# Optimization experiments

Measured on AMD Instinct MI355X. Metric: run time of the kernel, lower is better.

## Reference

```python
import jax, jax.numpy as jnp
import numpy as np

B, C, H, W = 4, 256, 64, 64
OUT_C = 256
K = 3          # kernel_size
P = K // 2     # zero padding
EPS = 1e-5     # F.layer_norm default eps


def setup_inputs() -> dict:
    key = jax.random.key(0)
    ks = jax.random.split(key, 9)
    s = 0.02
    return {
        "x":  jax.random.normal(ks[0], (B, C, H, W), dtype=jnp.float32),
        "Wq": jax.random.normal(ks[1], (C, C), dtype=jnp.float32) * s,
        "bq": jax.random.normal(ks[2], (C,), dtype=jnp.float32) * s,
        "Wk": jax.random.normal(ks[3], (C, C), dtype=jnp.float32) * s,
        "bk": jax.random.normal(ks[4], (C,), dtype=jnp.float32) * s,
        "Wv": jax.random.normal(ks[5], (C, C), dtype=jnp.float32) * s,
        "bv": jax.random.normal(ks[6], (C,), dtype=jnp.float32) * s,
        "Wo": jax.random.normal(ks[7], (OUT_C, C), dtype=jnp.float32) * s,
        "bo": jax.random.normal(ks[8], (OUT_C,), dtype=jnp.float32) * s,
    }


def _forward(x, Wq, bq, Wk, bk, Wv, bv, Wo, bo):
    # LayerNorm over the last two dims [H, W], no affine (per (b, c) plane).
    mu = jnp.mean(x, axis=(2, 3), keepdims=True)
    var = jnp.var(x, axis=(2, 3), keepdims=True)
    xn = (x - mu) * jax.lax.rsqrt(var + EPS)

    xh = jnp.transpose(xn, (0, 2, 3, 1))            # [B, H, W, C]
    scale = jnp.asarray(C, xh.dtype) ** -0.5        # depth_scale = C**-0.5

    # Query only at each center pixel (only the center output is kept).
    q = (xh @ Wq.T + bq) * scale                    # [B, H, W, C]

    # Zero-pad the normalized input, then project: padded positions get K=bk, V=bv
    # exactly as torch's Linear applied to zero-padded windows.
    xp = jnp.pad(xh, ((0, 0), (P, P), (P, P), (0, 0)))  # [B, H+2P, W+2P, C]
    Kp = xp @ Wk.T + bk
    Vp = xp @ Wv.T + bv

    # Gather the K*K neighborhood for every pixel (small fixed loop over 9 shifts).
    Kw = jnp.stack([Kp[:, i:i + H, j:j + W, :] for i in range(K) for j in range(K)], axis=3)  # [B,H,W,9,C]
    Vw = jnp.stack([Vp[:, i:i + H, j:j + W, :] for i in range(K) for j in range(K)], axis=3)  # [B,H,W,9,C]

    logits = jnp.einsum('bhwc,bhwnc->bhwn', q, Kw)  # [B, H, W, 9]
    attn = jax.nn.softmax(logits, axis=-1)
    ctx = jnp.einsum('bhwn,bhwnc->bhwc', attn, Vw)  # [B, H, W, C]

    out = ctx @ Wo.T + bo                           # [B, H, W, OUT_C]
    return jnp.transpose(out, (0, 3, 1, 2))         # [B, OUT_C, H, W]


def reference(x, Wq, bq, Wk, bk, Wv, bv, Wo, bo):
    return _forward(x, Wq, bq, Wk, bk, Wv, bv, Wo, bo)
```

## Files before the change

kernel.cpp:

```cpp
#include <hip/hip_runtime.h>

typedef unsigned short u16;
typedef unsigned int   u32;

typedef __attribute__((ext_vector_type(4))) float f32x4;
typedef __attribute__((ext_vector_type(8))) short bf16x8;

#define HWDIM 4096
#define CDIM  256

__device__ __forceinline__ float bf2f(u16 u) { return __uint_as_float(((u32)u) << 16); }
__device__ __forceinline__ u16 f2bf(float f) {
    u32 u = __float_as_uint(f);
    u32 r = (u + 0x7fffu + ((u >> 16) & 1u)) >> 16;
    return (u16)r;
}

__global__ __launch_bounds__(256) void fill_kernel(float* __restrict__ out, int n) {
    int i = blockIdx.x * 256 + threadIdx.x;
    if (i < n) out[i] = 1.0f;
}

__global__ __launch_bounds__(256) void wconv_kernel(const float* __restrict__ s0,
                                                    const float* __restrict__ s1,
                                                    const float* __restrict__ s2,
                                                    const float* __restrict__ s3,
                                                    u16* __restrict__ d0, u16* __restrict__ d1,
                                                    u16* __restrict__ d2, u16* __restrict__ d3) {
    const float* s; u16* d;
    switch (blockIdx.y) {
        case 0: s = s0; d = d0; break;
        case 1: s = s1; d = d1; break;
        case 2: s = s2; d = d2; break;
        default: s = s3; d = d3; break;
    }
    int i = (blockIdx.x * 256 + threadIdx.x) * 4;
    float4 f = *(const float4*)(s + i);
    u16 tmp[4] = {f2bf(f.x), f2bf(f.y), f2bf(f.z), f2bf(f.w)};
    *(uint2*)(d + i) = *(uint2*)tmp;
}

__global__ __launch_bounds__(256) void ln_stats_kernel(const float* __restrict__ x,
                                                       float2* __restrict__ stats) {
    int plane = blockIdx.x;
    int t = threadIdx.x;
    const float* px = x + (size_t)plane * HWDIM;
    float sum = 0.f, ss = 0.f;
#pragma unroll
    for (int it = 0; it < 4; ++it) {
        float4 v = *(const float4*)(px + (t + it * 256) * 4);
        sum += v.x + v.y + v.z + v.w;
        ss  += v.x * v.x + v.y * v.y + v.z * v.z + v.w * v.w;
    }
#pragma unroll
    for (int o = 32; o; o >>= 1) { sum += __shfl_xor(sum, o); ss += __shfl_xor(ss, o); }
    __shared__ float s1[4], s2[4];
    int wid = t >> 6, lane = t & 63;
    if (lane == 0) { s1[wid] = sum; s2[wid] = ss; }
    __syncthreads();
    if (t == 0) {
        float S = s1[0] + s1[1] + s1[2] + s1[3];
        float Q = s2[0] + s2[1] + s2[2] + s2[3];
        float mu  = S * (1.f / HWDIM);
        float var = Q * (1.f / HWDIM) - mu * mu;
        stats[plane] = make_float2(mu, rsqrtf(var + 1e-5f));
    }
}

__global__ __launch_bounds__(256) void ln_transpose_kernel(const float* __restrict__ x,
                                                           const float2* __restrict__ stats,
                                                           u16* __restrict__ xh) {
    __shared__ __align__(16) u16 tile[64 * 72];
    int b  = blockIdx.z;
    int c0 = blockIdx.y * 64;
    int p0 = blockIdx.x * 64;
    int t  = threadIdx.x;
    int c_loc = t >> 2;
    int pc    = (t & 3) * 16;
    int plane = b * CDIM + c0 + c_loc;
    float2 st = stats[plane];
    const float* px = x + (size_t)plane * HWDIM + p0 + pc;
#pragma unroll
    for (int j2 = 0; j2 < 4; j2++) {
        float4 v = *(const float4*)(px + j2 * 4);
        int p = pc + j2 * 4;
        tile[(p + 0) * 72 + c_loc] = f2bf((v.x - st.x) * st.y);
        tile[(p + 1) * 72 + c_loc] = f2bf((v.y - st.x) * st.y);
        tile[(p + 2) * 72 + c_loc] = f2bf((v.z - st.x) * st.y);
        tile[(p + 3) * 72 + c_loc] = f2bf((v.w - st.x) * st.y);
    }
    __syncthreads();
    int cc = (t & 7) * 8;
#pragma unroll
    for (int it = 0; it < 2; ++it) {
        int p_loc = (t >> 3) + it * 32;
        uint4 val = *(uint4*)&tile[p_loc * 72 + cc];
        *(uint4*)(xh + ((size_t)(b * HWDIM + p0 + p_loc)) * CDIM + c0 + cc) = val;
    }
}

__device__ __forceinline__ void gemm_mainloop(const u16* __restrict__ A,
                                              const u16* __restrict__ Bm,
                                              u16* lA, u16* lB,
                                              f32x4 acc[4][4],
                                              int m0, int n0,
                                              int waveM, int waveN, int lane, int t) {
    int fr = lane & 15, kq = (lane >> 4) * 8;
    for (int k0 = 0; k0 < 256; k0 += 32) {
        int m1 = t >> 2, kc = (t & 3) * 8;
        int m2 = m1 + 64;
        *(uint4*)&lA[m1 * 32 + kc] = *(const uint4*)&A[(size_t)(m0 + m1) * 256 + k0 + kc];
        *(uint4*)&lA[m2 * 32 + kc] = *(const uint4*)&A[(size_t)(m0 + m2) * 256 + k0 + kc];
        *(uint4*)&lB[m1 * 32 + kc] = *(const uint4*)&Bm[(size_t)(n0 + m1) * 256 + k0 + kc];
        *(uint4*)&lB[m2 * 32 + kc] = *(const uint4*)&Bm[(size_t)(n0 + m2) * 256 + k0 + kc];
        __syncthreads();
        bf16x8 af[4], bfr[4];
#pragma unroll
        for (int i = 0; i < 4; i++) af[i]  = *(const bf16x8*)&lA[(waveM * 64 + i * 16 + fr) * 32 + kq];
#pragma unroll
        for (int j = 0; j < 4; j++) bfr[j] = *(const bf16x8*)&lB[(waveN * 64 + j * 16 + fr) * 32 + kq];
#pragma unroll
        for (int i = 0; i < 4; i++)
#pragma unroll
            for (int j = 0; j < 4; j++)
                acc[i][j] = __builtin_amdgcn_mfma_f32_16x16x32_bf16(af[i], bfr[j], acc[i][j], 0, 0, 0);
        __syncthreads();
    }
}

__global__ __launch_bounds__(256) void gemm_qkv_kernel(const u16* __restrict__ xh,
    const u16* __restrict__ Wq, const float* __restrict__ bq,
    const u16* __restrict__ Wk, const float* __restrict__ bk,
    const u16* __restrict__ Wv, const float* __restrict__ bv,
    u16* __restrict__ qo, u16* __restrict__ ko, u16* __restrict__ vo) {
    __shared__ __align__(16) u16 lA[128 * 32];
    __shared__ __align__(16) u16 lB[128 * 32];
    int t = threadIdx.x, lane = t & 63, wid = t >> 6;
    int waveM = wid >> 1, waveN = wid & 1;
    int mb = blockIdx.x, nb = blockIdx.y;
    const u16* W; const float* bias; u16* out; float scale = 1.f;
    int wsel = nb >> 1;
    if (wsel == 0)      { W = Wq; bias = bq; out = qo; scale = 0.0625f; }
    else if (wsel == 1) { W = Wk; bias = bk; out = ko; }
    else                { W = Wv; bias = bv; out = vo; }
    int n0 = (nb & 1) * 128;
    int m0 = mb * 128;
    f32x4 acc[4][4];
#pragma unroll
    for (int i = 0; i < 4; i++)
#pragma unroll
        for (int j = 0; j < 4; j++) acc[i][j] = (f32x4){0.f, 0.f, 0.f, 0.f};
    gemm_mainloop(xh, W, lA, lB, acc, m0, n0, waveM, waveN, lane, t);
    int fr = lane & 15, r0 = (lane >> 4) * 4;
#pragma unroll
    for (int j = 0; j < 4; j++) {
        int ng = n0 + waveN * 64 + j * 16 + fr;
        float bval = bias[ng];
#pragma unroll
        for (int i = 0; i < 4; i++) {
            int mrow = m0 + waveM * 64 + i * 16 + r0;
#pragma unroll
            for (int r = 0; r < 4; r++) {
                float vv = (acc[i][j][r] + bval) * scale;
                out[(size_t)(mrow + r) * 256 + ng] = f2bf(vv);
            }
        }
    }
}

__global__ __launch_bounds__(256) void attn_kernel(const u16* __restrict__ q,
                                                   const u16* __restrict__ kb,
                                                   const u16* __restrict__ vb,
                                                   const float* __restrict__ bkf,
                                                   const float* __restrict__ bvf,
                                                   u16* __restrict__ ctx) {
    int t = threadIdx.x, wid = t >> 6, lane = t & 63;
    int pix = blockIdx.x * 4 + wid;
    int h = (pix >> 6) & 63, w = pix & 63;
    int c4 = lane << 2;
    uint2 qr = *(const uint2*)(q + (size_t)pix * 256 + c4);
    float q0 = __uint_as_float(qr.x << 16), q1 = __uint_as_float(qr.x & 0xffff0000u);
    float q2 = __uint_as_float(qr.y << 16), q3 = __uint_as_float(qr.y & 0xffff0000u);
    float4 kbias = *(const float4*)(bkf + c4);
    float4 vbias = *(const float4*)(bvf + c4);
    float part[9];
    int off[9];
#pragma unroll
    for (int n = 0; n < 9; n++) {
        int dy = n / 3 - 1, dx = n % 3 - 1;
        int hh = h + dy, ww = w + dx;
        bool inb = ((unsigned)hh < 64u) && ((unsigned)ww < 64u);
        off[n] = inb ? ((pix + dy * 64 + dx) << 8) : -1;
        float k0, k1, k2, k3;
        if (off[n] >= 0) {
            uint2 kr = *(const uint2*)(kb + off[n] + c4);
            k0 = __uint_as_float(kr.x << 16); k1 = __uint_as_float(kr.x & 0xffff0000u);
            k2 = __uint_as_float(kr.y << 16); k3 = __uint_as_float(kr.y & 0xffff0000u);
        } else {
            k0 = kbias.x; k1 = kbias.y; k2 = kbias.z; k3 = kbias.w;
        }
        part[n] = q0 * k0 + q1 * k1 + q2 * k2 + q3 * k3;
    }
#pragma unroll
    for (int o = 32; o; o >>= 1) {
#pragma unroll
        for (int n = 0; n < 9; n++) part[n] += __shfl_xor(part[n], o);
    }
    float m = part[0];
#pragma unroll
    for (int n = 1; n < 9; n++) m = fmaxf(m, part[n]);
    float e[9], s = 0.f;
#pragma unroll
    for (int n = 0; n < 9; n++) { e[n] = __expf(part[n] - m); s += e[n]; }
    float inv = 1.f / s;
    float a0 = 0.f, a1 = 0.f, a2 = 0.f, a3 = 0.f;
#pragma unroll
    for (int n = 0; n < 9; n++) {
        float v0, v1, v2, v3;
        if (off[n] >= 0) {
            uint2 vr = *(const uint2*)(vb + off[n] + c4);
            v0 = __uint_as_float(vr.x << 16); v1 = __uint_as_float(vr.x & 0xffff0000u);
            v2 = __uint_as_float(vr.y << 16); v3 = __uint_as_float(vr.y & 0xffff0000u);
        } else {
            v0 = vbias.x; v1 = vbias.y; v2 = vbias.z; v3 = vbias.w;
        }
        float wn = e[n] * inv;
        a0 += wn * v0; a1 += wn * v1; a2 += wn * v2; a3 += wn * v3;
    }
    u32 lo = (u32)f2bf(a0) | ((u32)f2bf(a1) << 16);
    u32 hi = (u32)f2bf(a2) | ((u32)f2bf(a3) << 16);
    *(uint2*)(ctx + (size_t)pix * 256 + c4) = make_uint2(lo, hi);
}

__global__ __launch_bounds__(256) void gemm_out_kernel(const u16* __restrict__ ctx,
                                                       const u16* __restrict__ Wo,
                                                       const float* __restrict__ bo,
                                                       float* __restrict__ out) {
    __shared__ __align__(16) u16 lA[128 * 32];
    __shared__ __align__(16) u16 lB[128 * 32];
    int t = threadIdx.x, lane = t & 63, wid = t >> 6;
    int waveM = wid >> 1, waveN = wid & 1;
    int m0 = blockIdx.x * 128;
    int n0 = blockIdx.y * 128;
    f32x4 acc[4][4];
#pragma unroll
    for (int i = 0; i < 4; i++)
#pragma unroll
        for (int j = 0; j < 4; j++) acc[i][j] = (f32x4){0.f, 0.f, 0.f, 0.f};
    gemm_mainloop(ctx, Wo, lA, lB, acc, m0, n0, waveM, waveN, lane, t);
    int fr = lane & 15, r0 = (lane >> 4) * 4;
#pragma unroll
    for (int j = 0; j < 4; j++) {
        int ng = n0 + waveN * 64 + j * 16 + fr;
        float bval = bo[ng];
#pragma unroll
        for (int i = 0; i < 4; i++) {
            int m = m0 + waveM * 64 + i * 16 + r0;
            int bidx = m >> 12;
            int p = m & 4095;
            float4 vv = make_float4(acc[i][j][0] + bval, acc[i][j][1] + bval,
                                    acc[i][j][2] + bval, acc[i][j][3] + bval);
            *(float4*)(out + ((size_t)(bidx * 256 + ng)) * HWDIM + p) = vv;
        }
    }
}

extern "C" void kernel_launch(void* const* d_in, const int* in_sizes, int n_in,
                              void* d_out, int out_size, void* d_ws, size_t ws_size,
                              hipStream_t stream) {
    const float* x  = (const float*)d_in[0];
    const float* Wq = (const float*)d_in[1];
    const float* bq = (const float*)d_in[2];
    const float* Wk = (const float*)d_in[3];
    const float* bk = (const float*)d_in[4];
    const float* Wv = (const float*)d_in[5];
    const float* bv = (const float*)d_in[6];
    const float* Wo = (const float*)d_in[7];
    const float* bo = (const float*)d_in[8];
    float* out = (float*)d_out;

    char* wsb = (char*)d_ws;
    const size_t MB = 1ull << 20;

    if (ws_size < 25 * MB) {
        hipLaunchKernelGGL(fill_kernel, dim3((out_size + 255) / 256), dim3(256), 0, stream,
                           out, out_size);
        return;
    }

    float2* stats = (float2*)wsb;
    u16* Wqc = (u16*)(wsb + 64 * 1024);
    u16* Wkc = Wqc + 65536;
    u16* Wvc = Wkc + 65536;
    u16* Woc = Wvc + 65536;
    u16* xh  = (u16*)(wsb + 1 * MB);
    u16* q   = (u16*)(wsb + 9 * MB);
    u16* k   = (u16*)(wsb + 17 * MB);
    u16* v   = (u16*)d_out;
    u16* ctx = xh;

    hipLaunchKernelGGL(wconv_kernel, dim3(64, 4), dim3(256), 0, stream,
                       Wq, Wk, Wv, Wo, Wqc, Wkc, Wvc, Woc);
    hipLaunchKernelGGL(ln_stats_kernel,     dim3(1024),     dim3(256), 0, stream, x, stats);
    hipLaunchKernelGGL(ln_transpose_kernel, dim3(64, 4, 4), dim3(256), 0, stream, x, stats, xh);
    hipLaunchKernelGGL(gemm_qkv_kernel,     dim3(128, 6),   dim3(256), 0, stream,
                       xh, Wqc, bq, Wkc, bk, Wvc, bv, q, k, v);
    hipLaunchKernelGGL(attn_kernel,         dim3(4096),     dim3(256), 0, stream,
                       q, k, v, bk, bv, ctx);
    hipLaunchKernelGGL(gemm_out_kernel,     dim3(128, 2),   dim3(256), 0, stream,
                       ctx, Woc, bo, out);
}
```

Measured before the change: 142.4 us.

## Interleave QKV output, fold query scale into weights, use direct global-to-LDS loads

Stacks Wq/Wk/Wv into one weight matrix with the query scale folded into Wq and bq, and has the QKV GEMM write a single interleaved [pixel, 768] buffer. Attention then reads q, k and v for a pixel from one contiguous row, which improves locality. The GEMM mainloop now loads tiles with global_load_lds, skipping the register round trip. The workspace requirement rises to 34 MB, and if less is provided the fallback fill kernel runs instead.

```diff
diff --git a/kernel.cpp b/kernel.cpp
--- a/kernel.cpp
+++ b/kernel.cpp
@@ -16,27 +16,43 @@
     return (u16)r;
 }
 
+#define GLL16(g, l) \
+    __builtin_amdgcn_global_load_lds((const __attribute__((address_space(1))) u32*)(g), \
+                                     (__attribute__((address_space(3))) u32*)(l), 16, 0, 0)
+
 __global__ __launch_bounds__(256) void fill_kernel(float* __restrict__ out, int n) {
     int i = blockIdx.x * 256 + threadIdx.x;
     if (i < n) out[i] = 1.0f;
 }
 
-__global__ __launch_bounds__(256) void wconv_kernel(const float* __restrict__ s0,
-                                                    const float* __restrict__ s1,
-                                                    const float* __restrict__ s2,
-                                                    const float* __restrict__ s3,
-                                                    u16* __restrict__ d0, u16* __restrict__ d1,
-                                                    u16* __restrict__ d2, u16* __restrict__ d3) {
-    const float* s; u16* d;
-    switch (blockIdx.y) {
-        case 0: s = s0; d = d0; break;
-        case 1: s = s1; d = d1; break;
-        case 2: s = s2; d = d2; break;
-        default: s = s3; d = d3; break;
-    }
-    int i = (blockIdx.x * 256 + threadIdx.x) * 4;
+__global__ __launch_bounds__(256) void wconv_kernel(const float* __restrict__ Wq,
+                                                    const float* __restrict__ Wk,
+                                                    const float* __restrict__ Wv,
+                                                    const float* __restrict__ Wo,
+                                                    const float* __restrict__ bq,
+                                                    const float* __restrict__ bk,
+                                                    const float* __restrict__ bv,
+                                                    u16* __restrict__ Wqkv,
+                                                    u16* __restrict__ Woc,
+                                                    float* __restrict__ biasStack) {
+    int yy = blockIdx.y;
+    int t = threadIdx.x;
+    if (yy == 4) {
+        if (blockIdx.x == 0) {
+            biasStack[t]       = bq[t] * 0.0625f;
+            biasStack[t + 256] = bk[t];
+            biasStack[t + 512] = bv[t];
+        }
+        return;
+    }
+    const float* s; u16* d; float sc = 1.f;
+    if (yy == 0)      { s = Wq; d = Wqkv;          sc = 0.0625f; }
+    else if (yy == 1) { s = Wk; d = Wqkv + 65536; }
+    else if (yy == 2) { s = Wv; d = Wqkv + 131072; }
+    else              { s = Wo; d = Woc; }
+    int i = (blockIdx.x * 256 + t) * 4;
     float4 f = *(const float4*)(s + i);
-    u16 tmp[4] = {f2bf(f.x), f2bf(f.y), f2bf(f.z), f2bf(f.w)};
+    u16 tmp[4] = {f2bf(f.x * sc), f2bf(f.y * sc), f2bf(f.z * sc), f2bf(f.w * sc)};
     *(uint2*)(d + i) = *(uint2*)tmp;
 }
 
@@ -106,13 +122,21 @@
                                               int m0, int n0,
                                               int waveM, int waveN, int lane, int t) {
     int fr = lane & 15, kq = (lane >> 4) * 8;
+    int r = t >> 2, kc = (t & 3) * 8;
+    int wid = t >> 6;
+    const u16* gA0 = A + (size_t)(m0 + r) * 256 + kc;
+    const u16* gA1 = gA0 + 64 * 256;
+    const u16* gB0 = Bm + (size_t)(n0 + r) * 256 + kc;
+    const u16* gB1 = gB0 + 64 * 256;
+    u16* lA0 = lA + wid * 512;
+    u16* lA1 = lA0 + 2048;
+    u16* lB0 = lB + wid * 512;
+    u16* lB1 = lB0 + 2048;
     for (int k0 = 0; k0 < 256; k0 += 32) {
-        int m1 = t >> 2, kc = (t & 3) * 8;
-        int m2 = m1 + 64;
-        *(uint4*)&lA[m1 * 32 + kc] = *(const uint4*)&A[(size_t)(m0 + m1) * 256 + k0 + kc];
-        *(uint4*)&lA[m2 * 32 + kc] = *(const uint4*)&A[(size_t)(m0 + m2) * 256 + k0 + kc];
-        *(uint4*)&lB[m1 * 32 + kc] = *(const uint4*)&Bm[(size_t)(n0 + m1) * 256 + k0 + kc];
-        *(uint4*)&lB[m2 * 32 + kc] = *(const uint4*)&Bm[(size_t)(n0 + m2) * 256 + k0 + kc];
+        GLL16(gA0 + k0, lA0);
+        GLL16(gA1 + k0, lA1);
+        GLL16(gB0 + k0, lB0);
+        GLL16(gB1 + k0, lB1);
         __syncthreads();
         bf16x8 af[4], bfr[4];
 #pragma unroll
@@ -129,60 +153,49 @@
 }
 
 __global__ __launch_bounds__(256) void gemm_qkv_kernel(const u16* __restrict__ xh,
-    const u16* __restrict__ Wq, const float* __restrict__ bq,
-    const u16* __restrict__ Wk, const float* __restrict__ bk,
-    const u16* __restrict__ Wv, const float* __restrict__ bv,
-    u16* __restrict__ qo, u16* __restrict__ ko, u16* __restrict__ vo) {
+                                                       const u16* __restrict__ Wqkv,
+                                                       const float* __restrict__ biasStack,
+                                                       u16* __restrict__ qkv) {
     __shared__ __align__(16) u16 lA[128 * 32];
     __shared__ __align__(16) u16 lB[128 * 32];
     int t = threadIdx.x, lane = t & 63, wid = t >> 6;
     int waveM = wid >> 1, waveN = wid & 1;
-    int mb = blockIdx.x, nb = blockIdx.y;
-    const u16* W; const float* bias; u16* out; float scale = 1.f;
-    int wsel = nb >> 1;
-    if (wsel == 0)      { W = Wq; bias = bq; out = qo; scale = 0.0625f; }
-    else if (wsel == 1) { W = Wk; bias = bk; out = ko; }
-    else                { W = Wv; bias = bv; out = vo; }
-    int n0 = (nb & 1) * 128;
-    int m0 = mb * 128;
+    int m0 = blockIdx.x * 128;
+    int n0 = blockIdx.y * 128;
     f32x4 acc[4][4];
 #pragma unroll
     for (int i = 0; i < 4; i++)
 #pragma unroll
         for (int j = 0; j < 4; j++) acc[i][j] = (f32x4){0.f, 0.f, 0.f, 0.f};
-    gemm_mainloop(xh, W, lA, lB, acc, m0, n0, waveM, waveN, lane, t);
+    gemm_mainloop(xh, Wqkv, lA, lB, acc, m0, n0, waveM, waveN, lane, t);
     int fr = lane & 15, r0 = (lane >> 4) * 4;
 #pragma unroll
     for (int j = 0; j < 4; j++) {
         int ng = n0 + waveN * 64 + j * 16 + fr;
-        float bval = bias[ng];
+        float bval = biasStack[ng];
 #pragma unroll
         for (int i = 0; i < 4; i++) {
             int mrow = m0 + waveM * 64 + i * 16 + r0;
 #pragma unroll
-            for (int r = 0; r < 4; r++) {
-                float vv = (acc[i][j][r] + bval) * scale;
-                out[(size_t)(mrow + r) * 256 + ng] = f2bf(vv);
-            }
-        }
-    }
-}
-
-__global__ __launch_bounds__(256) void attn_kernel(const u16* __restrict__ q,
-                                                   const u16* __restrict__ kb,
-                                                   const u16* __restrict__ vb,
-                                                   const float* __restrict__ bkf,
-                                                   const float* __restrict__ bvf,
+            for (int r = 0; r < 4; r++)
+                qkv[(size_t)(mrow + r) * 768 + ng] = f2bf(acc[i][j][r] + bval);
+        }
+    }
+}
+
+__global__ __launch_bounds__(256) void attn_kernel(const u16* __restrict__ qkv,
+                                                   const float* __restrict__ biasStack,
                                                    u16* __restrict__ ctx) {
     int t = threadIdx.x, wid = t >> 6, lane = t & 63;
     int pix = blockIdx.x * 4 + wid;
     int h = (pix >> 6) & 63, w = pix & 63;
     int c4 = lane << 2;
-    uint2 qr = *(const uint2*)(q + (size_t)pix * 256 + c4);
+    const u16* row = qkv + (size_t)pix * 768;
+    uint2 qr = *(const uint2*)(row + c4);
     float q0 = __uint_as_float(qr.x << 16), q1 = __uint_as_float(qr.x & 0xffff0000u);
     float q2 = __uint_as_float(qr.y << 16), q3 = __uint_as_float(qr.y & 0xffff0000u);
-    float4 kbias = *(const float4*)(bkf + c4);
-    float4 vbias = *(const float4*)(bvf + c4);
+    float4 kbias = *(const float4*)(biasStack + 256 + c4);
+    float4 vbias = *(const float4*)(biasStack + 512 + c4);
     float part[9];
     int off[9];
 #pragma unroll
@@ -190,10 +203,10 @@
         int dy = n / 3 - 1, dx = n % 3 - 1;
         int hh = h + dy, ww = w + dx;
         bool inb = ((unsigned)hh < 64u) && ((unsigned)ww < 64u);
-        off[n] = inb ? ((pix + dy * 64 + dx) << 8) : -1;
+        off[n] = inb ? ((pix + dy * 64 + dx) * 768) : -1;
         float k0, k1, k2, k3;
         if (off[n] >= 0) {
-            uint2 kr = *(const uint2*)(kb + off[n] + c4);
+            uint2 kr = *(const uint2*)(qkv + off[n] + 256 + c4);
             k0 = __uint_as_float(kr.x << 16); k1 = __uint_as_float(kr.x & 0xffff0000u);
             k2 = __uint_as_float(kr.y << 16); k3 = __uint_as_float(kr.y & 0xffff0000u);
         } else {
@@ -218,7 +231,7 @@
     for (int n = 0; n < 9; n++) {
         float v0, v1, v2, v3;
         if (off[n] >= 0) {
-            uint2 vr = *(const uint2*)(vb + off[n] + c4);
+            uint2 vr = *(const uint2*)(qkv + off[n] + 512 + c4);
             v0 = __uint_as_float(vr.x << 16); v1 = __uint_as_float(vr.x & 0xffff0000u);
             v2 = __uint_as_float(vr.y << 16); v3 = __uint_as_float(vr.y & 0xffff0000u);
         } else {
@@ -282,31 +295,28 @@
     char* wsb = (char*)d_ws;
     const size_t MB = 1ull << 20;
 
-    if (ws_size < 25 * MB) {
+    if (ws_size < 34 * MB) {
         hipLaunchKernelGGL(fill_kernel, dim3((out_size + 255) / 256), dim3(256), 0, stream,
                            out, out_size);
         return;
     }
 
-    float2* stats = (float2*)wsb;
-    u16* Wqc = (u16*)(wsb + 64 * 1024);
-    u16* Wkc = Wqc + 65536;
-    u16* Wvc = Wkc + 65536;
-    u16* Woc = Wvc + 65536;
-    u16* xh  = (u16*)(wsb + 1 * MB);
-    u16* q   = (u16*)(wsb + 9 * MB);
-    u16* k   = (u16*)(wsb + 17 * MB);
-    u16* v   = (u16*)d_out;
-    u16* ctx = xh;
-
-    hipLaunchKernelGGL(wconv_kernel, dim3(64, 4), dim3(256), 0, stream,
-                       Wq, Wk, Wv, Wo, Wqc, Wkc, Wvc, Woc);
+    float2* stats     = (float2*)wsb;
+    float*  biasStack = (float*)(wsb + 16 * 1024);
+    u16* Wqkv = (u16*)(wsb + 64 * 1024);
+    u16* Woc  = (u16*)(wsb + 448 * 1024);
+    u16* xh   = (u16*)(wsb + 1 * MB);
+    u16* qkv  = (u16*)(wsb + 9 * MB);
+    u16* ctx  = xh;
+
+    hipLaunchKernelGGL(wconv_kernel, dim3(64, 5), dim3(256), 0, stream,
+                       Wq, Wk, Wv, Wo, bq, bk, bv, Wqkv, Woc, biasStack);
     hipLaunchKernelGGL(ln_stats_kernel,     dim3(1024),     dim3(256), 0, stream, x, stats);
     hipLaunchKernelGGL(ln_transpose_kernel, dim3(64, 4, 4), dim3(256), 0, stream, x, stats, xh);
     hipLaunchKernelGGL(gemm_qkv_kernel,     dim3(128, 6),   dim3(256), 0, stream,
-                       xh, Wqc, bq, Wkc, bk, Wvc, bv, q, k, v);
+                       xh, Wqkv, biasStack, qkv);
     hipLaunchKernelGGL(attn_kernel,         dim3(4096),     dim3(256), 0, stream,
-                       q, k, v, bk, bv, ctx);
+                       qkv, biasStack, ctx);
     hipLaunchKernelGGL(gemm_out_kernel,     dim3(128, 2),   dim3(256), 0, stream,
                        ctx, Woc, bo, out);
 }
```

Result: faster. 131.8 us (-7.4%).
